# Optimization experiments

Hardware: AMD Instinct MI355X
Metric: run time of the kernel (lower is better)

## Reference

```python
import jax, jax.numpy as jnp
import numpy as np

P_X, P_H, P_L, P_VT, P_ET, B = 512, 1024, 4, 512, 256, 512
IN_DIM = P_X + 2 * P_H  # concat([x, prev_time_h, prev_layer_h])


def setup_inputs() -> dict:
    key = jax.random.key(0)
    ks = jax.random.split(key, 10)
    sc_in = 1.0 / np.sqrt(IN_DIM)
    sc_lh = 1.0 / np.sqrt(P_L * P_H)
    return {
        "input_x": jax.random.normal(ks[0], (B, P_X), jnp.float32),
        "h_prev": jax.random.normal(ks[1], (P_L, B, P_H), jnp.float32),
        "c_prev": jax.random.normal(ks[2], (P_L, B, P_H), jnp.float32),
        # stacked gate weights: [L, 4 gates (i,f,o,s), h, in_dim]
        "Wg": jax.random.uniform(ks[3], (P_L, 4, P_H, IN_DIM), jnp.float32, -sc_in, sc_in),
        "bg": jax.random.uniform(ks[4], (P_L, 4, P_H), jnp.float32, -sc_in, sc_in),
        "W_y": jax.random.uniform(ks[5], (P_VT, P_L * P_H), jnp.float32, -sc_lh, sc_lh),
        "b_y": jax.random.uniform(ks[6], (P_VT,), jnp.float32, -sc_lh, sc_lh),
        "W_E": jax.random.uniform(ks[7], (P_ET, P_L * P_H), jnp.float32, -sc_lh, sc_lh),
        "b_E": jax.random.uniform(ks[8], (P_ET,), jnp.float32, -sc_lh, sc_lh),
    }


def _controller(input_x, h_prev, c_prev, Wg, bg):
    prev_layer = jnp.zeros((input_x.shape[0], P_H), input_x.dtype)
    hiddens = []
    for i in range(P_L):  # loop over small fixed layer count
        z = jnp.concatenate([input_x, h_prev[i], prev_layer], axis=-1)  # [B, IN_DIM]
        g = jnp.einsum("bd,ghd->bgh", z, Wg[i]) + bg[i]  # [B, 4, H], one fused GEMM
        i_g = jax.nn.sigmoid(g[:, 0])
        f_g = jax.nn.sigmoid(g[:, 1])
        o_g = jax.nn.sigmoid(g[:, 2])
        s_g = jnp.tanh(g[:, 3])
        c_new = f_g * c_prev[i] + i_g * s_g
        h_new = o_g * jnp.tanh(c_new)
        hiddens.append(h_new)
        prev_layer = h_new
    return jnp.concatenate(hiddens, axis=-1)  # [B, L*H]


def reference(input_x, h_prev, c_prev, Wg, bg, W_y, b_y, W_E, b_E):
    hidden = _controller(input_x, h_prev, c_prev, Wg, bg)
    output = hidden @ W_y.T + b_y      # [B, v_t]
    interface = hidden @ W_E.T + b_E   # [B, E_t]
    return (output, interface)
```

## Files before the change

kernel.cpp:

```cpp
#include <hip/hip_runtime.h>


typedef short    shortx8  __attribute__((ext_vector_type(8)));
typedef float    floatx16 __attribute__((ext_vector_type(16)));

__device__ __forceinline__ unsigned int f2bf1(float x) {
  unsigned int u = __float_as_uint(x);
  return (u + 0x7fffu + ((u >> 16) & 1u)) >> 16;
}
__device__ __forceinline__ unsigned int f2bf2(float lo, float hi) {
  return f2bf1(lo) | (f2bf1(hi) << 16);
}
__device__ __forceinline__ float sigm(float x) { return 1.f / (1.f + __expf(-x)); }
__device__ __forceinline__ float tanh_(float x) { return 1.f - 2.f / (__expf(2.f * x) + 1.f); }

__global__ __launch_bounds__(256) void prep_a0(const float* __restrict__ x,
                                               const float* __restrict__ hp,
                                               unsigned short* __restrict__ A0) {
  const int l   = blockIdx.y;
  const int idx = blockIdx.x * 256 + threadIdx.x;
  const int b   = idx / 192;
  const int kk  = (idx - b * 192) * 8;
  float v[8];
  if (kk < 512) {
    const float* s = x + (size_t)b * 512 + kk;
#pragma unroll
    for (int i = 0; i < 8; ++i) v[i] = s[i];
  } else {
    const float* s = hp + ((size_t)l * 512 + b) * 1024 + (kk - 512);
#pragma unroll
    for (int i = 0; i < 8; ++i) v[i] = s[i];
  }
  uint4 o;
  o.x = f2bf2(v[0], v[1]); o.y = f2bf2(v[2], v[3]);
  o.z = f2bf2(v[4], v[5]); o.w = f2bf2(v[6], v[7]);
  *(uint4*)(A0 + ((size_t)l * 512 + b) * 1536 + kk) = o;
}

__global__ __launch_bounds__(256, 2) void gemm_gates(
    const unsigned short* __restrict__ A0, const float* __restrict__ Wg,
    const float* __restrict__ bg, float* __restrict__ G) {
  __shared__ __align__(16) unsigned short As[2][128 * 64];
  __shared__ __align__(16) unsigned short Bs[2][128 * 64];
  const int tid = threadIdx.x, lane = tid & 63, wave = tid >> 6;
  const int mbase = blockIdx.x * 128;
  const int nbase = blockIdx.y * 128;
  const int l     = blockIdx.z;
  const unsigned short* Ab = A0 + ((size_t)l * 512 + mbase) * 1536;
  const float*          Bb = Wg + (size_t)l * 4096 * 2560 + (size_t)nbase * 2560;
  const int arow = wave * 8 + (lane >> 3);
  const int akg  = lane & 7;

  uint4  apf[4];
  float4 bpf[8];
  auto loadT = [&](int kt) {
    const int kg = kt * 64;
#pragma unroll
    for (int r = 0; r < 4; ++r)
      apf[r] = *(const uint4*)(Ab + (size_t)(arow + r * 32) * 1536 + kg + akg * 8);
#pragma unroll
    for (int j = 0; j < 8; ++j) {
      const int idx = j * 256 + tid;
      bpf[j] = *(const float4*)(Bb + (size_t)(idx >> 4) * 2560 + kg + (idx & 15) * 4);
    }
  };
  auto storeT = [&](int buf) {
#pragma unroll
    for (int r = 0; r < 4; ++r) {
      const int row = arow + r * 32;
      *(uint4*)(&As[buf][row * 64 + ((akg ^ (row & 7)) * 8)]) = apf[r];
    }
#pragma unroll
    for (int j = 0; j < 8; ++j) {
      const int idx = j * 256 + tid;
      const int n = idx >> 4, kc = (idx & 15) * 4;
      uint2 pk;
      pk.x = f2bf2(bpf[j].x, bpf[j].y);
      pk.y = f2bf2(bpf[j].z, bpf[j].w);
      *(uint2*)(&Bs[buf][n * 64 + (((kc >> 3) ^ (n & 7)) * 8) + (kc & 4)]) = pk;
    }
  };

  floatx16 acc[2][2];
#pragma unroll
  for (int a = 0; a < 2; ++a)
#pragma unroll
    for (int b2 = 0; b2 < 2; ++b2)
#pragma unroll
      for (int r = 0; r < 16; ++r) acc[a][b2][r] = 0.f;

  const int wm = (wave >> 1) * 64, wn = (wave & 1) * 64;
  loadT(0);
  storeT(0);
  __syncthreads();
  for (int kt = 0; kt < 24; ++kt) {
    if (kt + 1 < 24) loadT(kt + 1);
    const int cb = kt & 1;
#pragma unroll
    for (int ks = 0; ks < 4; ++ks) {
      const int gb = ks * 2 + (lane >> 5);
      shortx8 af[2], bfv[2];
#pragma unroll
      for (int sm = 0; sm < 2; ++sm) {
        const int row = wm + sm * 32 + (lane & 31);
        af[sm] = *(const shortx8*)(&As[cb][row * 64 + ((gb ^ (row & 7)) * 8)]);
      }
#pragma unroll
      for (int sn = 0; sn < 2; ++sn) {
        const int row = wn + sn * 32 + (lane & 31);
        bfv[sn] = *(const shortx8*)(&Bs[cb][row * 64 + ((gb ^ (row & 7)) * 8)]);
      }
#pragma unroll
      for (int sm = 0; sm < 2; ++sm)
#pragma unroll
        for (int sn = 0; sn < 2; ++sn)
          acc[sm][sn] = __builtin_amdgcn_mfma_f32_32x32x16_bf16(
              af[sm], bfv[sn], acc[sm][sn], 0, 0, 0);
    }
    if (kt + 1 < 24) storeT((kt + 1) & 1);
    __syncthreads();
  }

  const float* bgl = bg + (size_t)l * 4096;
  float* Gl = G + ((size_t)l * 512 + mbase) * 4096;
#pragma unroll
  for (int sm = 0; sm < 2; ++sm)
#pragma unroll
    for (int sn = 0; sn < 2; ++sn) {
      const int col = nbase + wn + sn * 32 + (lane & 31);
      const float bias = bgl[col];
#pragma unroll
      for (int r = 0; r < 16; ++r) {
        const int row = wm + sm * 32 + ((r & 3) + 8 * (r >> 2) + 4 * (lane >> 5));
        Gl[(size_t)row * 4096 + col] = acc[sm][sn][r] + bias;
      }
    }
}

__global__ __launch_bounds__(256) void cell0(const float* __restrict__ G,
                                             const float* __restrict__ cp_l,
                                             unsigned short* __restrict__ hidden) {
  const int idx = (blockIdx.x * 256 + threadIdx.x) * 4;
  const int b = idx >> 10, h = idx & 1023;
  const float* g0 = G + (size_t)b * 4096;
  const float4 vi = *(const float4*)(g0 + h);
  const float4 vf = *(const float4*)(g0 + 1024 + h);
  const float4 vo = *(const float4*)(g0 + 2048 + h);
  const float4 vs = *(const float4*)(g0 + 3072 + h);
  const float4 cp = *(const float4*)(cp_l + (size_t)b * 1024 + h);
  const float gi[4] = {vi.x, vi.y, vi.z, vi.w};
  const float gf[4] = {vf.x, vf.y, vf.z, vf.w};
  const float go[4] = {vo.x, vo.y, vo.z, vo.w};
  const float gs[4] = {vs.x, vs.y, vs.z, vs.w};
  const float cc[4] = {cp.x, cp.y, cp.z, cp.w};
  float hn[4];
#pragma unroll
  for (int j = 0; j < 4; ++j) {
    const float c = sigm(gf[j]) * cc[j] + sigm(gi[j]) * tanh_(gs[j]);
    hn[j] = sigm(go[j]) * tanh_(c);
  }
  uint2 o;
  o.x = f2bf2(hn[0], hn[1]);
  o.y = f2bf2(hn[2], hn[3]);
  *(uint2*)(hidden + (size_t)b * 4096 + h) = o;
}

__global__ __launch_bounds__(512, 2) void gemm_seq_cell(
    const unsigned short* __restrict__ hidden_ro, const float* __restrict__ Wg,
    const float* __restrict__ G, const float* __restrict__ c_prev,
    unsigned short* __restrict__ hidden_w, int l) {
  __shared__ __align__(16) unsigned char raw[49152];
  unsigned short* As = (unsigned short*)raw;
  unsigned short* Bs = (unsigned short*)(raw + 32768);
  float*          Gex = (float*)raw;
  const int tid = threadIdx.x, lane = tid & 63, wave = tid >> 6;
  const int mbase = blockIdx.x * 128;
  const int h0    = blockIdx.y * 16;
  const unsigned short* Ab = hidden_ro + (size_t)(l - 1) * 1024;
  const float*          Bl = Wg + (size_t)l * 4096 * 2560 + 1536;

  uint4  apf[2];
  float4 bpf[2];
  auto loadT = [&](int kt) {
    const int kg = kt * 64;
#pragma unroll
    for (int r = 0; r < 2; ++r) {
      const int row = (tid >> 3) + r * 64;
      apf[r] = *(const uint4*)(Ab + (size_t)(mbase + row) * 4096 + kg + (tid & 7) * 8);
    }
#pragma unroll
    for (int j = 0; j < 2; ++j) {
      const int idx = j * 512 + tid;
      const int nl = idx >> 4, kc = (idx & 15) * 4;
      const int grow = (nl >> 4) * 1024 + h0 + (nl & 15);
      bpf[j] = *(const float4*)(Bl + (size_t)grow * 2560 + kg + kc);
    }
  };
  auto storeT = [&](int buf) {
#pragma unroll
    for (int r = 0; r < 2; ++r) {
      const int row = (tid >> 3) + r * 64;
      *(uint4*)(&As[buf * 8192 + row * 64 + (((tid & 7) ^ (row & 7)) * 8)]) = apf[r];
    }
#pragma unroll
    for (int j = 0; j < 2; ++j) {
      const int idx = j * 512 + tid;
      const int nl = idx >> 4, kc = (idx & 15) * 4;
      uint2 pk;
      pk.x = f2bf2(bpf[j].x, bpf[j].y);
      pk.y = f2bf2(bpf[j].z, bpf[j].w);
      *(uint2*)(&Bs[buf * 4096 + nl * 64 + (((kc >> 3) ^ (nl & 7)) * 8) + (kc & 4)]) = pk;
    }
  };

  floatx16 acc;
#pragma unroll
  for (int r = 0; r < 16; ++r) acc[r] = 0.f;
  const int wm = (wave & 3) * 32, wn = (wave >> 2) * 32;

  loadT(0);
  storeT(0);
  __syncthreads();
  for (int kt = 0; kt < 16; ++kt) {
    if (kt + 1 < 16) loadT(kt + 1);
    const int cb = kt & 1;
    const int rowa = wm + (lane & 31);
    const int rowb = wn + (lane & 31);
#pragma unroll
    for (int ks = 0; ks < 4; ++ks) {
      const int gb = ks * 2 + (lane >> 5);
      const shortx8 af = *(const shortx8*)(&As[cb * 8192 + rowa * 64 + ((gb ^ (rowa & 7)) * 8)]);
      const shortx8 bfv = *(const shortx8*)(&Bs[cb * 4096 + rowb * 64 + ((gb ^ (rowb & 7)) * 8)]);
      acc = __builtin_amdgcn_mfma_f32_32x32x16_bf16(af, bfv, acc, 0, 0, 0);
    }
    if (kt + 1 < 16) storeT((kt + 1) & 1);
    __syncthreads();
  }

  {
    const int col = wn + (lane & 31);
#pragma unroll
    for (int r = 0; r < 16; ++r) {
      const int row = wm + ((r & 3) + 8 * (r >> 2) + 4 * (lane >> 5));
      Gex[row * 65 + col] = acc[r];
    }
  }
  __syncthreads();

  const int hh = tid & 15, q = tid >> 4;
#pragma unroll
  for (int bi = 0; bi < 4; ++bi) {
    const int bl = bi * 32 + q;
    const int b  = mbase + bl;
    const int hg = h0 + hh;
    const float* Gb = G + ((size_t)l * 512 + b) * 4096;
    float gv[4];
#pragma unroll
    for (int g = 0; g < 4; ++g)
      gv[g] = Gex[bl * 65 + g * 16 + hh] + Gb[g * 1024 + hg];
    const float c_old = c_prev[((size_t)l * 512 + b) * 1024 + hg];
    const float c  = sigm(gv[1]) * c_old + sigm(gv[0]) * tanh_(gv[3]);
    const float hn = sigm(gv[2]) * tanh_(c);
    hidden_w[(size_t)b * 4096 + l * 1024 + hg] = (unsigned short)f2bf1(hn);
  }
}

__global__ __launch_bounds__(256) void gemm_heads(
    const unsigned short* __restrict__ A, const float* __restrict__ Wy,
    const float* __restrict__ WE, float* __restrict__ Cp) {
  __shared__ __align__(16) unsigned short As[2][128 * 64];
  __shared__ __align__(16) unsigned short Bs[2][128 * 64];
  const int tid = threadIdx.x, lane = tid & 63, wave = tid >> 6;
  const int mbase = blockIdx.z * 128;
  const int nt    = blockIdx.y;
  const int nbase = nt * 128;
  const float* Bb = (nt < 4) ? (Wy + (size_t)nbase * 4096)
                             : (WE + (size_t)(nbase - 512) * 4096);
  const int k0 = blockIdx.x * 512;
  const unsigned short* Ab = A + (size_t)mbase * 4096;
  const int arow = wave * 8 + (lane >> 3);
  const int akg  = lane & 7;

  uint4  apf[4];
  float4 bpf[8];
  auto loadT = [&](int kt) {
    const int kg = k0 + kt * 64;
#pragma unroll
    for (int r = 0; r < 4; ++r)
      apf[r] = *(const uint4*)(Ab + (size_t)(arow + r * 32) * 4096 + kg + akg * 8);
#pragma unroll
    for (int j = 0; j < 8; ++j) {
      const int idx = j * 256 + tid;
      bpf[j] = *(const float4*)(Bb + (size_t)(idx >> 4) * 4096 + kg + (idx & 15) * 4);
    }
  };
  auto storeT = [&](int buf) {
#pragma unroll
    for (int r = 0; r < 4; ++r) {
      const int row = arow + r * 32;
      *(uint4*)(&As[buf][row * 64 + ((akg ^ (row & 7)) * 8)]) = apf[r];
    }
#pragma unroll
    for (int j = 0; j < 8; ++j) {
      const int idx = j * 256 + tid;
      const int n = idx >> 4, kc = (idx & 15) * 4;
      uint2 pk;
      pk.x = f2bf2(bpf[j].x, bpf[j].y);
      pk.y = f2bf2(bpf[j].z, bpf[j].w);
      *(uint2*)(&Bs[buf][n * 64 + (((kc >> 3) ^ (n & 7)) * 8) + (kc & 4)]) = pk;
    }
  };

  floatx16 acc[2][2];
#pragma unroll
  for (int a = 0; a < 2; ++a)
#pragma unroll
    for (int b2 = 0; b2 < 2; ++b2)
#pragma unroll
      for (int r = 0; r < 16; ++r) acc[a][b2][r] = 0.f;
  const int wm = (wave >> 1) * 64, wn = (wave & 1) * 64;

  loadT(0);
  storeT(0);
  __syncthreads();
  for (int kt = 0; kt < 8; ++kt) {
    if (kt + 1 < 8) loadT(kt + 1);
    const int cb = kt & 1;
#pragma unroll
    for (int ks = 0; ks < 4; ++ks) {
      const int gb = ks * 2 + (lane >> 5);
      shortx8 af[2], bfv[2];
#pragma unroll
      for (int sm = 0; sm < 2; ++sm) {
        const int row = wm + sm * 32 + (lane & 31);
        af[sm] = *(const shortx8*)(&As[cb][row * 64 + ((gb ^ (row & 7)) * 8)]);
      }
#pragma unroll
      for (int sn = 0; sn < 2; ++sn) {
        const int row = wn + sn * 32 + (lane & 31);
        bfv[sn] = *(const shortx8*)(&Bs[cb][row * 64 + ((gb ^ (row & 7)) * 8)]);
      }
#pragma unroll
      for (int sm = 0; sm < 2; ++sm)
#pragma unroll
        for (int sn = 0; sn < 2; ++sn)
          acc[sm][sn] = __builtin_amdgcn_mfma_f32_32x32x16_bf16(
              af[sm], bfv[sn], acc[sm][sn], 0, 0, 0);
    }
    if (kt + 1 < 8) storeT((kt + 1) & 1);
    __syncthreads();
  }

  float* Co = Cp + (size_t)blockIdx.x * 512 * 768;
#pragma unroll
  for (int sm = 0; sm < 2; ++sm)
#pragma unroll
    for (int sn = 0; sn < 2; ++sn) {
      const int col = nbase + wn + sn * 32 + (lane & 31);
#pragma unroll
      for (int r = 0; r < 16; ++r) {
        const int row = mbase + wm + sm * 32 +
                        ((r & 3) + 8 * (r >> 2) + 4 * (lane >> 5));
        Co[(size_t)row * 768 + col] = acc[sm][sn][r];
      }
    }
}

__global__ __launch_bounds__(256) void head_reduce(
    const float* __restrict__ hp, const float* __restrict__ b_y,
    const float* __restrict__ b_E, float* __restrict__ out) {
  const int n = blockIdx.x * 256 + threadIdx.x;
  const int b = blockIdx.y;
  float s = 0.f;
#pragma unroll
  for (int ks = 0; ks < 8; ++ks)
    s += hp[(size_t)ks * 512 * 768 + (size_t)b * 768 + n];
  if (n < 512)
    out[(size_t)b * 512 + n] = s + b_y[n];
  else
    out[(size_t)512 * 512 + (size_t)b * 256 + (n - 512)] = s + b_E[n - 512];
}

extern "C" void kernel_launch(void* const* d_in, const int* in_sizes, int n_in,
                              void* d_out, int out_size, void* d_ws, size_t ws_size,
                              hipStream_t stream) {
  const float* x      = (const float*)d_in[0];
  const float* h_prev = (const float*)d_in[1];
  const float* c_prev = (const float*)d_in[2];
  const float* Wg     = (const float*)d_in[3];
  const float* bg     = (const float*)d_in[4];
  const float* W_y    = (const float*)d_in[5];
  const float* b_y    = (const float*)d_in[6];
  const float* W_E    = (const float*)d_in[7];
  const float* b_E    = (const float*)d_in[8];

  char* ws = (char*)d_ws;
  unsigned short* A0     = (unsigned short*)(ws + 0);
  float*          G      = (float*)(ws + 6291456);
  unsigned short* hidden = (unsigned short*)(ws + 39845888);
  float*          hpart  = (float*)(ws + 44040192);

  prep_a0<<<dim3(384, 4), 256, 0, stream>>>(x, h_prev, A0);
  gemm_gates<<<dim3(4, 32, 4), 256, 0, stream>>>(A0, Wg, bg, G);
  cell0<<<512, 256, 0, stream>>>(G, c_prev, hidden);
  for (int l = 1; l < 4; ++l)
    gemm_seq_cell<<<dim3(4, 64), 512, 0, stream>>>(hidden, Wg, G, c_prev,
                                                   hidden, l);
  gemm_heads<<<dim3(8, 6, 4), 256, 0, stream>>>(hidden, W_y, W_E, hpart);
  head_reduce<<<dim3(3, 512), 256, 0, stream>>>(hpart, b_y, b_E, (float*)d_out);
}
```

Before: 404.9 us.

## Shrink GEMM tiles, add XCD-aware block mapping, split-K sequential layers with separate cell kernel

All three GEMM kernels move to smaller tiles (64-wide N, or 64x64) with a single LDS buffer, drop double-buffering, and raise occupancy to 4 blocks per CU. A 1D grid remaps block ids so neighbouring tiles land on the same XCD. The sequential layers now use a 2-way split-K GEMM that writes partial sums to scratch, followed by a separate elementwise cell kernel, replacing the fused GEMM+cell kernel. The aim is more blocks in flight and better L2 locality, at the cost of losing load/compute overlap, extra scratch traffic and extra launches per layer.

New measurement: 523.7 us. 1.29x slower.

```diff
diff --git a/kernel.cpp b/kernel.cpp
--- a/kernel.cpp
+++ b/kernel.cpp
@@ -37,103 +37,79 @@
   *(uint4*)(A0 + ((size_t)l * 512 + b) * 1536 + kk) = o;
 }
 
-__global__ __launch_bounds__(256, 2) void gemm_gates(
+__global__ __launch_bounds__(256, 4) void gemm_gates(
     const unsigned short* __restrict__ A0, const float* __restrict__ Wg,
     const float* __restrict__ bg, float* __restrict__ G) {
-  __shared__ __align__(16) unsigned short As[2][128 * 64];
-  __shared__ __align__(16) unsigned short Bs[2][128 * 64];
+  __shared__ __align__(16) unsigned short As[128 * 64];
+  __shared__ __align__(16) unsigned short Bs[64 * 64];
   const int tid = threadIdx.x, lane = tid & 63, wave = tid >> 6;
-  const int mbase = blockIdx.x * 128;
-  const int nbase = blockIdx.y * 128;
-  const int l     = blockIdx.z;
+  const int id  = blockIdx.x;
+  const int xcd = id & 7, j = id >> 3;
+  const int mt  = j & 3, rest = j >> 2;
+  const int c   = xcd * 32 + rest;
+  const int l   = c >> 6, nt = c & 63;
+  const int mbase = mt * 128, nbase = nt * 64;
   const unsigned short* Ab = A0 + ((size_t)l * 512 + mbase) * 1536;
   const float*          Bb = Wg + (size_t)l * 4096 * 2560 + (size_t)nbase * 2560;
-  const int arow = wave * 8 + (lane >> 3);
-  const int akg  = lane & 7;
-
-  uint4  apf[4];
-  float4 bpf[8];
-  auto loadT = [&](int kt) {
+  const int arow = tid >> 3;
+  const int akg  = tid & 7;
+
+  floatx16 acc[2];
+#pragma unroll
+  for (int r = 0; r < 16; ++r) { acc[0][r] = 0.f; acc[1][r] = 0.f; }
+  const int wm = (wave >> 1) * 64, wn = (wave & 1) * 32;
+
+  for (int kt = 0; kt < 24; ++kt) {
     const int kg = kt * 64;
+    uint4 av[4];
 #pragma unroll
     for (int r = 0; r < 4; ++r)
-      apf[r] = *(const uint4*)(Ab + (size_t)(arow + r * 32) * 1536 + kg + akg * 8);
-#pragma unroll
-    for (int j = 0; j < 8; ++j) {
-      const int idx = j * 256 + tid;
-      bpf[j] = *(const float4*)(Bb + (size_t)(idx >> 4) * 2560 + kg + (idx & 15) * 4);
-    }
-  };
-  auto storeT = [&](int buf) {
+      av[r] = *(const uint4*)(Ab + (size_t)(arow + r * 32) * 1536 + kg + akg * 8);
+    float4 bv[4];
+#pragma unroll
+    for (int u = 0; u < 4; ++u) {
+      const int idx = u * 256 + tid;
+      bv[u] = *(const float4*)(Bb + (size_t)(idx >> 4) * 2560 + kg + (idx & 15) * 4);
+    }
+    __syncthreads();
 #pragma unroll
     for (int r = 0; r < 4; ++r) {
       const int row = arow + r * 32;
-      *(uint4*)(&As[buf][row * 64 + ((akg ^ (row & 7)) * 8)]) = apf[r];
-    }
-#pragma unroll
-    for (int j = 0; j < 8; ++j) {
-      const int idx = j * 256 + tid;
+      *(uint4*)(&As[row * 64 + ((akg ^ (row & 7)) * 8)]) = av[r];
+    }
+#pragma unroll
+    for (int u = 0; u < 4; ++u) {
+      const int idx = u * 256 + tid;
       const int n = idx >> 4, kc = (idx & 15) * 4;
       uint2 pk;
-      pk.x = f2bf2(bpf[j].x, bpf[j].y);
-      pk.y = f2bf2(bpf[j].z, bpf[j].w);
-      *(uint2*)(&Bs[buf][n * 64 + (((kc >> 3) ^ (n & 7)) * 8) + (kc & 4)]) = pk;
-    }
-  };
-
-  floatx16 acc[2][2];
-#pragma unroll
-  for (int a = 0; a < 2; ++a)
-#pragma unroll
-    for (int b2 = 0; b2 < 2; ++b2)
-#pragma unroll
-      for (int r = 0; r < 16; ++r) acc[a][b2][r] = 0.f;
-
-  const int wm = (wave >> 1) * 64, wn = (wave & 1) * 64;
-  loadT(0);
-  storeT(0);
-  __syncthreads();
-  for (int kt = 0; kt < 24; ++kt) {
-    if (kt + 1 < 24) loadT(kt + 1);
-    const int cb = kt & 1;
+      pk.x = f2bf2(bv[u].x, bv[u].y);
+      pk.y = f2bf2(bv[u].z, bv[u].w);
+      *(uint2*)(&Bs[n * 64 + (((kc >> 3) ^ (n & 7)) * 8) + (kc & 4)]) = pk;
+    }
+    __syncthreads();
 #pragma unroll
     for (int ks = 0; ks < 4; ++ks) {
       const int gb = ks * 2 + (lane >> 5);
-      shortx8 af[2], bfv[2];
+      const int rowb = wn + (lane & 31);
+      const shortx8 bfv = *(const shortx8*)(&Bs[rowb * 64 + ((gb ^ (rowb & 7)) * 8)]);
 #pragma unroll
       for (int sm = 0; sm < 2; ++sm) {
-        const int row = wm + sm * 32 + (lane & 31);
-        af[sm] = *(const shortx8*)(&As[cb][row * 64 + ((gb ^ (row & 7)) * 8)]);
+        const int rowa = wm + sm * 32 + (lane & 31);
+        const shortx8 af = *(const shortx8*)(&As[rowa * 64 + ((gb ^ (rowa & 7)) * 8)]);
+        acc[sm] = __builtin_amdgcn_mfma_f32_32x32x16_bf16(af, bfv, acc[sm], 0, 0, 0);
       }
-#pragma unroll
-      for (int sn = 0; sn < 2; ++sn) {
-        const int row = wn + sn * 32 + (lane & 31);
-        bfv[sn] = *(const shortx8*)(&Bs[cb][row * 64 + ((gb ^ (row & 7)) * 8)]);
-      }
-#pragma unroll
-      for (int sm = 0; sm < 2; ++sm)
-#pragma unroll
-        for (int sn = 0; sn < 2; ++sn)
-          acc[sm][sn] = __builtin_amdgcn_mfma_f32_32x32x16_bf16(
-              af[sm], bfv[sn], acc[sm][sn], 0, 0, 0);
-    }
-    if (kt + 1 < 24) storeT((kt + 1) & 1);
-    __syncthreads();
-  }
-
-  const float* bgl = bg + (size_t)l * 4096;
+    }
+  }
+
+  const int col = nbase + wn + (lane & 31);
+  const float bias = bg[(size_t)l * 4096 + col];
   float* Gl = G + ((size_t)l * 512 + mbase) * 4096;
 #pragma unroll
   for (int sm = 0; sm < 2; ++sm)
 #pragma unroll
-    for (int sn = 0; sn < 2; ++sn) {
-      const int col = nbase + wn + sn * 32 + (lane & 31);
-      const float bias = bgl[col];
-#pragma unroll
-      for (int r = 0; r < 16; ++r) {
-        const int row = wm + sm * 32 + ((r & 3) + 8 * (r >> 2) + 4 * (lane >> 5));
-        Gl[(size_t)row * 4096 + col] = acc[sm][sn][r] + bias;
-      }
+    for (int r = 0; r < 16; ++r) {
+      const int row = wm + sm * 32 + ((r & 3) + 8 * (r >> 2) + 4 * (lane >> 5));
+      Gl[(size_t)row * 4096 + col] = acc[sm][r] + bias;
     }
 }
 
@@ -155,9 +131,9 @@
   const float cc[4] = {cp.x, cp.y, cp.z, cp.w};
   float hn[4];
 #pragma unroll
-  for (int j = 0; j < 4; ++j) {
-    const float c = sigm(gf[j]) * cc[j] + sigm(gi[j]) * tanh_(gs[j]);
-    hn[j] = sigm(go[j]) * tanh_(c);
+  for (int jj = 0; jj < 4; ++jj) {
+    const float c = sigm(gf[jj]) * cc[jj] + sigm(gi[jj]) * tanh_(gs[jj]);
+    hn[jj] = sigm(go[jj]) * tanh_(c);
   }
   uint2 o;
   o.x = f2bf2(hn[0], hn[1]);
@@ -165,205 +141,180 @@
   *(uint2*)(hidden + (size_t)b * 4096 + h) = o;
 }
 
-__global__ __launch_bounds__(512, 2) void gemm_seq_cell(
+__global__ __launch_bounds__(256, 4) void gemm_seq(
     const unsigned short* __restrict__ hidden_ro, const float* __restrict__ Wg,
-    const float* __restrict__ G, const float* __restrict__ c_prev,
-    unsigned short* __restrict__ hidden_w, int l) {
-  __shared__ __align__(16) unsigned char raw[49152];
-  unsigned short* As = (unsigned short*)raw;
-  unsigned short* Bs = (unsigned short*)(raw + 32768);
-  float*          Gex = (float*)raw;
+    float* __restrict__ P, int l) {
+  __shared__ __align__(16) unsigned short As[64 * 64];
+  __shared__ __align__(16) unsigned short Bs[64 * 64];
   const int tid = threadIdx.x, lane = tid & 63, wave = tid >> 6;
-  const int mbase = blockIdx.x * 128;
-  const int h0    = blockIdx.y * 16;
+  const int id  = blockIdx.x;
+  const int xcd = id & 7, j = id >> 3;
+  const int mt  = j & 7, rest = j >> 3;
+  const int c   = xcd * 16 + rest;
+  const int nt  = c & 63, ks0 = c >> 6;
+  const int mbase = mt * 64, nbase = nt * 64;
+  const int k0 = ks0 * 512;
   const unsigned short* Ab = hidden_ro + (size_t)(l - 1) * 1024;
-  const float*          Bl = Wg + (size_t)l * 4096 * 2560 + 1536;
-
-  uint4  apf[2];
-  float4 bpf[2];
-  auto loadT = [&](int kt) {
-    const int kg = kt * 64;
+  const float* Bb = Wg + (size_t)l * 4096 * 2560 + 1536 + (size_t)nbase * 2560;
+  const int arow = tid >> 3;
+  const int akg  = tid & 7;
+
+  floatx16 acc;
+#pragma unroll
+  for (int r = 0; r < 16; ++r) acc[r] = 0.f;
+  const int wm = (wave & 1) * 32, wn = (wave >> 1) * 32;
+
+  for (int kt = 0; kt < 8; ++kt) {
+    const int kg = k0 + kt * 64;
+    uint4 av[2];
+#pragma unroll
+    for (int r = 0; r < 2; ++r)
+      av[r] = *(const uint4*)(Ab + (size_t)(mbase + arow + r * 32) * 4096 + kg + akg * 8);
+    float4 bv[4];
+#pragma unroll
+    for (int u = 0; u < 4; ++u) {
+      const int idx = u * 256 + tid;
+      bv[u] = *(const float4*)(Bb + (size_t)(idx >> 4) * 2560 + kg + (idx & 15) * 4);
+    }
+    __syncthreads();
 #pragma unroll
     for (int r = 0; r < 2; ++r) {
-      const int row = (tid >> 3) + r * 64;
-      apf[r] = *(const uint4*)(Ab + (size_t)(mbase + row) * 4096 + kg + (tid & 7) * 8);
-    }
-#pragma unroll
-    for (int j = 0; j < 2; ++j) {
-      const int idx = j * 512 + tid;
-      const int nl = idx >> 4, kc = (idx & 15) * 4;
-      const int grow = (nl >> 4) * 1024 + h0 + (nl & 15);
-      bpf[j] = *(const float4*)(Bl + (size_t)grow * 2560 + kg + kc);
-    }
-  };
-  auto storeT = [&](int buf) {
-#pragma unroll
-    for (int r = 0; r < 2; ++r) {
-      const int row = (tid >> 3) + r * 64;
-      *(uint4*)(&As[buf * 8192 + row * 64 + (((tid & 7) ^ (row & 7)) * 8)]) = apf[r];
-    }
-#pragma unroll
-    for (int j = 0; j < 2; ++j) {
-      const int idx = j * 512 + tid;
-      const int nl = idx >> 4, kc = (idx & 15) * 4;
+      const int row = arow + r * 32;
+      *(uint4*)(&As[row * 64 + ((akg ^ (row & 7)) * 8)]) = av[r];
+    }
+#pragma unroll
+    for (int u = 0; u < 4; ++u) {
+      const int idx = u * 256 + tid;
+      const int n = idx >> 4, kc = (idx & 15) * 4;
       uint2 pk;
-      pk.x = f2bf2(bpf[j].x, bpf[j].y);
-      pk.y = f2bf2(bpf[j].z, bpf[j].w);
-      *(uint2*)(&Bs[buf * 4096 + nl * 64 + (((kc >> 3) ^ (nl & 7)) * 8) + (kc & 4)]) = pk;
-    }
-  };
-
-  floatx16 acc;
-#pragma unroll
-  for (int r = 0; r < 16; ++r) acc[r] = 0.f;
-  const int wm = (wave & 3) * 32, wn = (wave >> 2) * 32;
-
-  loadT(0);
-  storeT(0);
-  __syncthreads();
-  for (int kt = 0; kt < 16; ++kt) {
-    if (kt + 1 < 16) loadT(kt + 1);
-    const int cb = kt & 1;
-    const int rowa = wm + (lane & 31);
-    const int rowb = wn + (lane & 31);
+      pk.x = f2bf2(bv[u].x, bv[u].y);
+      pk.y = f2bf2(bv[u].z, bv[u].w);
+      *(uint2*)(&Bs[n * 64 + (((kc >> 3) ^ (n & 7)) * 8) + (kc & 4)]) = pk;
+    }
+    __syncthreads();
 #pragma unroll
     for (int ks = 0; ks < 4; ++ks) {
       const int gb = ks * 2 + (lane >> 5);
-      const shortx8 af = *(const shortx8*)(&As[cb * 8192 + rowa * 64 + ((gb ^ (rowa & 7)) * 8)]);
-      const shortx8 bfv = *(const shortx8*)(&Bs[cb * 4096 + rowb * 64 + ((gb ^ (rowb & 7)) * 8)]);
+      const int rowa = wm + (lane & 31);
+      const int rowb = wn + (lane & 31);
+      const shortx8 af  = *(const shortx8*)(&As[rowa * 64 + ((gb ^ (rowa & 7)) * 8)]);
+      const shortx8 bfv = *(const shortx8*)(&Bs[rowb * 64 + ((gb ^ (rowb & 7)) * 8)]);
       acc = __builtin_amdgcn_mfma_f32_32x32x16_bf16(af, bfv, acc, 0, 0, 0);
     }
-    if (kt + 1 < 16) storeT((kt + 1) & 1);
-    __syncthreads();
-  }
-
-  {
-    const int col = wn + (lane & 31);
-#pragma unroll
-    for (int r = 0; r < 16; ++r) {
-      const int row = wm + ((r & 3) + 8 * (r >> 2) + 4 * (lane >> 5));
-      Gex[row * 65 + col] = acc[r];
-    }
-  }
-  __syncthreads();
-
-  const int hh = tid & 15, q = tid >> 4;
-#pragma unroll
-  for (int bi = 0; bi < 4; ++bi) {
-    const int bl = bi * 32 + q;
-    const int b  = mbase + bl;
-    const int hg = h0 + hh;
-    const float* Gb = G + ((size_t)l * 512 + b) * 4096;
-    float gv[4];
-#pragma unroll
-    for (int g = 0; g < 4; ++g)
-      gv[g] = Gex[bl * 65 + g * 16 + hh] + Gb[g * 1024 + hg];
-    const float c_old = c_prev[((size_t)l * 512 + b) * 1024 + hg];
-    const float c  = sigm(gv[1]) * c_old + sigm(gv[0]) * tanh_(gv[3]);
-    const float hn = sigm(gv[2]) * tanh_(c);
-    hidden_w[(size_t)b * 4096 + l * 1024 + hg] = (unsigned short)f2bf1(hn);
-  }
-}
-
-__global__ __launch_bounds__(256) void gemm_heads(
+  }
+
+  float* Co = P + (size_t)ks0 * 512 * 4096;
+  const int col = nbase + wn + (lane & 31);
+#pragma unroll
+  for (int r = 0; r < 16; ++r) {
+    const int row = mbase + wm + ((r & 3) + 8 * (r >> 2) + 4 * (lane >> 5));
+    Co[(size_t)row * 4096 + col] = acc[r];
+  }
+}
+
+__global__ __launch_bounds__(256) void cell_seq(
+    const float* __restrict__ P, const float* __restrict__ G_l,
+    const float* __restrict__ cp_l, unsigned short* __restrict__ hidden, int l) {
+  const int idx = (blockIdx.x * 256 + threadIdx.x) * 4;
+  const int b = idx >> 10, h = idx & 1023;
+  const float* p0 = P + (size_t)b * 4096;
+  const float* p1 = P + (size_t)512 * 4096 + (size_t)b * 4096;
+  const float* g0 = G_l + (size_t)b * 4096;
+  float gv[4][4];
+#pragma unroll
+  for (int g = 0; g < 4; ++g) {
+    const float4 a = *(const float4*)(p0 + g * 1024 + h);
+    const float4 bb = *(const float4*)(p1 + g * 1024 + h);
+    const float4 cg = *(const float4*)(g0 + g * 1024 + h);
+    gv[g][0] = a.x + bb.x + cg.x;
+    gv[g][1] = a.y + bb.y + cg.y;
+    gv[g][2] = a.z + bb.z + cg.z;
+    gv[g][3] = a.w + bb.w + cg.w;
+  }
+  const float4 cp = *(const float4*)(cp_l + (size_t)b * 1024 + h);
+  const float cc[4] = {cp.x, cp.y, cp.z, cp.w};
+  float hn[4];
+#pragma unroll
+  for (int jj = 0; jj < 4; ++jj) {
+    const float c = sigm(gv[1][jj]) * cc[jj] + sigm(gv[0][jj]) * tanh_(gv[3][jj]);
+    hn[jj] = sigm(gv[2][jj]) * tanh_(c);
+  }
+  uint2 o;
+  o.x = f2bf2(hn[0], hn[1]);
+  o.y = f2bf2(hn[2], hn[3]);
+  *(uint2*)(hidden + (size_t)b * 4096 + l * 1024 + h) = o;
+}
+
+__global__ __launch_bounds__(256, 4) void gemm_heads(
     const unsigned short* __restrict__ A, const float* __restrict__ Wy,
-    const float* __restrict__ WE, float* __restrict__ Cp) {
-  __shared__ __align__(16) unsigned short As[2][128 * 64];
-  __shared__ __align__(16) unsigned short Bs[2][128 * 64];
+    const float* __restrict__ WE, float* __restrict__ P) {
+  __shared__ __align__(16) unsigned short As[64 * 64];
+  __shared__ __align__(16) unsigned short Bs[64 * 64];
   const int tid = threadIdx.x, lane = tid & 63, wave = tid >> 6;
-  const int mbase = blockIdx.z * 128;
-  const int nt    = blockIdx.y;
-  const int nbase = nt * 128;
-  const float* Bb = (nt < 4) ? (Wy + (size_t)nbase * 4096)
+  const int id  = blockIdx.x;
+  const int xcd = id & 7, j = id >> 3;
+  const int mt  = j & 7, rest = j >> 3;
+  const int c   = xcd * 12 + rest;
+  const int nt  = c % 12, ks0 = c / 12;
+  const int mbase = mt * 64, nbase = nt * 64;
+  const int k0 = ks0 * 512;
+  const float* Bb = (nt < 8) ? (Wy + (size_t)nbase * 4096)
                              : (WE + (size_t)(nbase - 512) * 4096);
-  const int k0 = blockIdx.x * 512;
-  const unsigned short* Ab = A + (size_t)mbase * 4096;
-  const int arow = wave * 8 + (lane >> 3);
-  const int akg  = lane & 7;
-
-  uint4  apf[4];
-  float4 bpf[8];
-  auto loadT = [&](int kt) {
+  const unsigned short* Ab = A;
+  const int arow = tid >> 3;
+  const int akg  = tid & 7;
+
+  floatx16 acc;
+#pragma unroll
+  for (int r = 0; r < 16; ++r) acc[r] = 0.f;
+  const int wm = (wave & 1) * 32, wn = (wave >> 1) * 32;
+
+  for (int kt = 0; kt < 8; ++kt) {
     const int kg = k0 + kt * 64;
-#pragma unroll
-    for (int r = 0; r < 4; ++r)
-      apf[r] = *(const uint4*)(Ab + (size_t)(arow + r * 32) * 4096 + kg + akg * 8);
-#pragma unroll
-    for (int j = 0; j < 8; ++j) {
-      const int idx = j * 256 + tid;
-      bpf[j] = *(const float4*)(Bb + (size_t)(idx >> 4) * 4096 + kg + (idx & 15) * 4);
-    }
-  };
-  auto storeT = [&](int buf) {
-#pragma unroll
-    for (int r = 0; r < 4; ++r) {
+    uint4 av[2];
+#pragma unroll
+    for (int r = 0; r < 2; ++r)
+      av[r] = *(const uint4*)(Ab + (size_t)(mbase + arow + r * 32) * 4096 + kg + akg * 8);
+    float4 bv[4];
+#pragma unroll
+    for (int u = 0; u < 4; ++u) {
+      const int idx = u * 256 + tid;
+      bv[u] = *(const float4*)(Bb + (size_t)(idx >> 4) * 4096 + kg + (idx & 15) * 4);
+    }
+    __syncthreads();
+#pragma unroll
+    for (int r = 0; r < 2; ++r) {
       const int row = arow + r * 32;
-      *(uint4*)(&As[buf][row * 64 + ((akg ^ (row & 7)) * 8)]) = apf[r];
-    }
-#pragma unroll
-    for (int j = 0; j < 8; ++j) {
-      const int idx = j * 256 + tid;
+      *(uint4*)(&As[row * 64 + ((akg ^ (row & 7)) * 8)]) = av[r];
+    }
+#pragma unroll
+    for (int u = 0; u < 4; ++u) {
+      const int idx = u * 256 + tid;
       const int n = idx >> 4, kc = (idx & 15) * 4;
       uint2 pk;
-      pk.x = f2bf2(bpf[j].x, bpf[j].y);
-      pk.y = f2bf2(bpf[j].z, bpf[j].w);
-      *(uint2*)(&Bs[buf][n * 64 + (((kc >> 3) ^ (n & 7)) * 8) + (kc & 4)]) = pk;
-    }
-  };
-
-  floatx16 acc[2][2];
-#pragma unroll
-  for (int a = 0; a < 2; ++a)
-#pragma unroll
-    for (int b2 = 0; b2 < 2; ++b2)
-#pragma unroll
-      for (int r = 0; r < 16; ++r) acc[a][b2][r] = 0.f;
-  const int wm = (wave >> 1) * 64, wn = (wave & 1) * 64;
-
-  loadT(0);
-  storeT(0);
-  __syncthreads();
-  for (int kt = 0; kt < 8; ++kt) {
-    if (kt + 1 < 8) loadT(kt + 1);
-    const int cb = kt & 1;
+      pk.x = f2bf2(bv[u].x, bv[u].y);
+      pk.y = f2bf2(bv[u].z, bv[u].w);
+      *(uint2*)(&Bs[n * 64 + (((kc >> 3) ^ (n & 7)) * 8) + (kc & 4)]) = pk;
+    }
+    __syncthreads();
 #pragma unroll
     for (int ks = 0; ks < 4; ++ks) {
       const int gb = ks * 2 + (lane >> 5);
-      shortx8 af[2], bfv[2];
-#pragma unroll
-      for (int sm = 0; sm < 2; ++sm) {
-        const int row = wm + sm * 32 + (lane & 31);
-        af[sm] = *(const shortx8*)(&As[cb][row * 64 + ((gb ^ (row & 7)) * 8)]);
-      }
-#pragma unroll
-      for (int sn = 0; sn < 2; ++sn) {
-        const int row = wn + sn * 32 + (lane & 31);
-        bfv[sn] = *(const shortx8*)(&Bs[cb][row * 64 + ((gb ^ (row & 7)) * 8)]);
-      }
-#pragma unroll
-      for (int sm = 0; sm < 2; ++sm)
-#pragma unroll
-        for (int sn = 0; sn < 2; ++sn)
-          acc[sm][sn] = __builtin_amdgcn_mfma_f32_32x32x16_bf16(
-              af[sm], bfv[sn], acc[sm][sn], 0, 0, 0);
-    }
-    if (kt + 1 < 8) storeT((kt + 1) & 1);
-    __syncthreads();
-  }
-
-  float* Co = Cp + (size_t)blockIdx.x * 512 * 768;
-#pragma unroll
-  for (int sm = 0; sm < 2; ++sm)
-#pragma unroll
-    for (int sn = 0; sn < 2; ++sn) {
-      const int col = nbase + wn + sn * 32 + (lane & 31);
-#pragma unroll
-      for (int r = 0; r < 16; ++r) {
-        const int row = mbase + wm + sm * 32 +
-                        ((r & 3) + 8 * (r >> 2) + 4 * (lane >> 5));
-        Co[(size_t)row * 768 + col] = acc[sm][sn][r];
-      }
-    }
+      const int rowa = wm + (lane & 31);
+      const int rowb = wn + (lane & 31);
+      const shortx8 af  = *(const shortx8*)(&As[rowa * 64 + ((gb ^ (rowa & 7)) * 8)]);
+      const shortx8 bfv = *(const shortx8*)(&Bs[rowb * 64 + ((gb ^ (rowb & 7)) * 8)]);
+      acc = __builtin_amdgcn_mfma_f32_32x32x16_bf16(af, bfv, acc, 0, 0, 0);
+    }
+  }
+
+  float* Co = P + (size_t)ks0 * 512 * 768;
+  const int col = nbase + wn + (lane & 31);
+#pragma unroll
+  for (int r = 0; r < 16; ++r) {
+    const int row = mbase + wm + ((r & 3) + 8 * (r >> 2) + 4 * (lane >> 5));
+    Co[(size_t)row * 768 + col] = acc[r];
+  }
 }
 
 __global__ __launch_bounds__(256) void head_reduce(
@@ -395,17 +346,19 @@
   const float* b_E    = (const float*)d_in[8];
 
   char* ws = (char*)d_ws;
-  unsigned short* A0     = (unsigned short*)(ws + 0);
-  float*          G      = (float*)(ws + 6291456);
-  unsigned short* hidden = (unsigned short*)(ws + 39845888);
-  float*          hpart  = (float*)(ws + 44040192);
+  unsigned short* A0      = (unsigned short*)(ws + 0);
+  float*          G       = (float*)(ws + 6291456);
+  unsigned short* hidden  = (unsigned short*)(ws + 39845888);
+  float*          scratch = (float*)(ws + 44040192);
 
   prep_a0<<<dim3(384, 4), 256, 0, stream>>>(x, h_prev, A0);
-  gemm_gates<<<dim3(4, 32, 4), 256, 0, stream>>>(A0, Wg, bg, G);
+  gemm_gates<<<1024, 256, 0, stream>>>(A0, Wg, bg, G);
   cell0<<<512, 256, 0, stream>>>(G, c_prev, hidden);
-  for (int l = 1; l < 4; ++l)
-    gemm_seq_cell<<<dim3(4, 64), 512, 0, stream>>>(hidden, Wg, G, c_prev,
-                                                   hidden, l);
-  gemm_heads<<<dim3(8, 6, 4), 256, 0, stream>>>(hidden, W_y, W_E, hpart);
-  head_reduce<<<dim3(3, 512), 256, 0, stream>>>(hpart, b_y, b_E, (float*)d_out);
-}
+  for (int l = 1; l < 4; ++l) {
+    gemm_seq<<<1024, 256, 0, stream>>>(hidden, Wg, scratch, l);
+    cell_seq<<<512, 256, 0, stream>>>(scratch, G + (size_t)l * 512 * 4096,
+                                      c_prev + (size_t)l * 512 * 1024, hidden, l);
+  }
+  gemm_heads<<<768, 256, 0, stream>>>(hidden, W_y, W_E, scratch);
+  head_reduce<<<dim3(3, 512), 256, 0, stream>>>(scratch, b_y, b_E, (float*)d_out);
+}
```
